# Kernel tuning notes

Measured on AMD Instinct MI355X. Metric: run time of the kernel, lower is better.

## Reference

```python
import jax, jax.numpy as jnp
import numpy as np

WINDOW = 128  # local attention window (non-overlapping blocks)
LN_EPS = 1e-5


def setup_inputs() -> dict:
    key = jax.random.key(0)
    ks = jax.random.split(key, 7)
    B, S, D = 8, 8192, 128
    scale = 1.0 / np.sqrt(D)
    x = jax.random.normal(ks[0], (B, S, D), dtype=jnp.float32)
    Wq = jax.random.normal(ks[1], (D, D), dtype=jnp.float32) * scale
    Wk = jax.random.normal(ks[2], (D, D), dtype=jnp.float32) * scale
    Wv = jax.random.normal(ks[3], (D, D), dtype=jnp.float32) * scale
    Wo = jax.random.normal(ks[4], (D, D), dtype=jnp.float32) * scale
    gamma = jnp.ones((D,), dtype=jnp.float32)
    beta = jnp.zeros((D,), dtype=jnp.float32)
    return {"x": x, "Wq": Wq, "Wk": Wk, "Wv": Wv, "Wo": Wo,
            "gamma": gamma, "beta": beta}


def _local_attention(xc, Wq, Wk, Wv, Wo):
    # xc: [B, L, D]; non-overlapping block-local attention, window=WINDOW
    B, L, D = xc.shape
    nb = L // WINDOW
    q = (xc @ Wq).reshape(B, nb, WINDOW, D)
    k = (xc @ Wk).reshape(B, nb, WINDOW, D)
    v = (xc @ Wv).reshape(B, nb, WINDOW, D)
    scores = jnp.einsum('bnwd,bnud->bnwu', q, k) / jnp.sqrt(
        jnp.asarray(D, xc.dtype))
    attn = jax.nn.softmax(scores, axis=-1)
    out = jnp.einsum('bnwu,bnud->bnwd', attn, v).reshape(B, L, D)
    return out @ Wo


def reference(x, Wq, Wk, Wv, Wo, gamma, beta):
    # passer starts as zeros_like(x); concat along seq dim doubles length
    xc = jnp.concatenate([x, jnp.zeros_like(x)], axis=1)  # [B, 2S, D]
    h = _local_attention(xc, Wq, Wk, Wv, Wo)
    # LayerNorm over last dim (learned affine)
    mu = jnp.mean(h, axis=-1, keepdims=True)
    var = jnp.mean(jnp.square(h - mu), axis=-1, keepdims=True)
    y = (h - mu) * jax.lax.rsqrt(var + LN_EPS) * gamma + beta
    # torch nn.GELU default is exact (erf) variant
    return jax.nn.gelu(y, approximate=False)
```

## Files before the change

kernel.cpp:

```cpp
#include <hip/hip_runtime.h>
#include <hip/hip_bf16.h>
#include <math.h>

using bf16 = __hip_bfloat16;
typedef short short8 __attribute__((ext_vector_type(8)));
typedef short short4v __attribute__((ext_vector_type(4)));
typedef float f32x4 __attribute__((ext_vector_type(4)));

#define MFMA16 __builtin_amdgcn_mfma_f32_16x16x32_bf16
#define S_ 8192

__device__ __forceinline__ int sw(int r, int chunk) {
  return r * 256 + (((chunk) ^ (r & 15)) << 4);
}

__device__ __forceinline__ float gelu_exact(float y) {
  return 0.5f * y * (1.0f + erff(y * 0.70710678118654752f));
}

__device__ __forceinline__ unsigned pack2(float a, float b) {
  unsigned ra = (unsigned)__bfloat16_as_ushort(__float2bfloat16(a));
  unsigned rb = (unsigned)__bfloat16_as_ushort(__float2bfloat16(b));
  return ra | (rb << 16);
}

__global__ void transw(const float* __restrict__ wq, const float* __restrict__ wk,
                       const float* __restrict__ wv, const float* __restrict__ wo,
                       bf16* __restrict__ wt) {
  __shared__ float smf[128 * 33];
  int m = blockIdx.x >> 2, sl = blockIdx.x & 3;
  const float* W = (m == 0) ? wq : (m == 1) ? wk : (m == 2) ? wv : wo;
  for (int i = 0; i < 4; ++i) {
    int u = threadIdx.x + i * 256;
    int k = u >> 3, cg = u & 7;
    float4 v = *(const float4*)(W + k * 128 + sl * 32 + cg * 4);
    smf[k * 33 + cg * 4 + 0] = v.x;
    smf[k * 33 + cg * 4 + 1] = v.y;
    smf[k * 33 + cg * 4 + 2] = v.z;
    smf[k * 33 + cg * 4 + 3] = v.w;
  }
  __syncthreads();
  for (int i = 0; i < 2; ++i) {
    int f = threadIdx.x + i * 256;
    int l15 = f & 15, q = (f >> 4) & 3, t = (f >> 6) & 3, ctl = (f >> 8) & 1;
    int ct = sl * 2 + ctl;
    int gf = ((ct * 4 + t) * 4 + q) * 16 + l15;
    int k0 = t * 32 + q * 8, nl = ctl * 16 + l15;
    bf16 tmp[8];
#pragma unroll
    for (int j = 0; j < 8; ++j)
      tmp[j] = __float2bfloat16(smf[(k0 + j) * 33 + nl]);
    *(uint4*)(wt + m * 16384 + gf * 8) = *(const uint4*)tmp;
  }
}

__device__ __forceinline__ void clr8(f32x4 acc[8]) {
#pragma unroll
  for (int j = 0; j < 8; ++j) acc[j] = (f32x4){0.f, 0.f, 0.f, 0.f};
}

__device__ __forceinline__ void mm_g(const char* tA, const char* wB, int row0,
                                     int l15, int quad, f32x4 acc[8]) {
  short8 a[4];
#pragma unroll
  for (int t = 0; t < 4; ++t)
    a[t] = *(const short8*)(tA + sw(row0 + l15, 4 * t + quad));
#pragma unroll
  for (int t = 0; t < 4; ++t) {
    short8 b[8];
#pragma unroll
    for (int ct = 0; ct < 8; ++ct)
      b[ct] = *(const short8*)(wB + ((((ct * 4 + t) * 4 + quad) * 16 + l15) << 4));
#pragma unroll
    for (int ct = 0; ct < 8; ++ct)
      acc[ct] = MFMA16(a[t], b[ct], acc[ct], 0, 0, 0);
  }
}

__device__ __forceinline__ void mm_l(const char* tA, const char* tB, int row0,
                                     int l15, int quad, f32x4 acc[8]) {
  short8 a[4];
#pragma unroll
  for (int t = 0; t < 4; ++t)
    a[t] = *(const short8*)(tA + sw(row0 + l15, 4 * t + quad));
#pragma unroll
  for (int t = 0; t < 4; ++t) {
    short8 b[8];
#pragma unroll
    for (int ct = 0; ct < 8; ++ct)
      b[ct] = *(const short8*)(tB + sw(ct * 16 + l15, 4 * t + quad));
#pragma unroll
    for (int ct = 0; ct < 8; ++ct)
      acc[ct] = MFMA16(a[t], b[ct], acc[ct], 0, 0, 0);
  }
}

__device__ __forceinline__ void store_strip(char* tile, int row0, int l15, int quad,
                                            const f32x4 acc[8], const float* rs) {
#pragma unroll
  for (int ct = 0; ct < 8; ++ct) {
    int col = ct * 16 + l15;
#pragma unroll
    for (int r = 0; r < 4; ++r) {
      int row = row0 + quad * 4 + r;
      float v = acc[ct][r];
      if (rs) v *= rs[r];
      *(bf16*)(tile + sw(row, col >> 3) + (col & 7) * 2) = __float2bfloat16(v);
    }
  }
}

__device__ __forceinline__ void stage_x_strip(char* strip, const float* xg, int lane) {
#pragma unroll
  for (int it = 0; it < 8; ++it) {
    int e = it * 256 + lane * 4;
    float4 f = *(const float4*)(xg + e);
    union { unsigned u[2]; short4v s; } pk;
    pk.u[0] = pack2(f.x, f.y);
    pk.u[1] = pack2(f.z, f.w);
    int r = e >> 7, chunk = (e >> 3) & 15, half = (lane & 1) * 8;
    *(short4v*)(strip + sw(r, chunk) + half) = pk.s;
  }
  asm volatile("" ::: "memory");
}

__global__ __launch_bounds__(512, 2) void attn_fused(
    const float* __restrict__ x, const bf16* __restrict__ wt,
    const float* __restrict__ gamma, const float* __restrict__ beta,
    float* __restrict__ out) {
  __shared__ uint4 ldsbuf[4096];
  char* t_x = (char*)ldsbuf;
  char* t_k = t_x + 32768;

  const int tid = threadIdx.x;
  const int wave = tid >> 6, lane = tid & 63;
  const int l15 = lane & 15, quad = lane >> 4;
  const int row0 = wave << 4;
  const int b = blockIdx.x >> 6, blk = blockIdx.x & 63;
  const float* xb = x + ((size_t)b * S_ + (size_t)blk * 128) * 128;
  float* outb = out + ((size_t)b * 2 * S_ + (size_t)blk * 128) * 128;

  {
    float* o2 = out + ((size_t)b * 2 * S_ + (size_t)(S_ + blk * 128)) * 128;
    int c0 = (tid * 4) & 127;
    float4 bv = *(const float4*)(beta + c0);
    float4 gv;
    gv.x = gelu_exact(bv.x); gv.y = gelu_exact(bv.y);
    gv.z = gelu_exact(bv.z); gv.w = gelu_exact(bv.w);
#pragma unroll
    for (int j = 0; j < 8; ++j)
      *(float4*)(o2 + tid * 4 + j * 2048) = gv;
  }

  stage_x_strip(t_x + wave * 4096, xb + (size_t)row0 * 128, lane);

  f32x4 acc[8];
  unsigned pV[16];

  clr8(acc);
  mm_g(t_x, (const char*)(wt + 16384), row0, l15, quad, acc);
  store_strip(t_k, row0, l15, quad, acc, nullptr);

  clr8(acc);
  mm_g(t_x, (const char*)(wt + 2 * 16384), row0, l15, quad, acc);
#pragma unroll
  for (int ct = 0; ct < 8; ++ct) {
    pV[2 * ct]     = pack2(acc[ct][0], acc[ct][1]);
    pV[2 * ct + 1] = pack2(acc[ct][2], acc[ct][3]);
  }

  clr8(acc);
  mm_g(t_x, (const char*)(wt + 0), row0, l15, quad, acc);
  store_strip(t_x, row0, l15, quad, acc, nullptr);
  __syncthreads();

  clr8(acc);
  mm_l(t_x, t_k, row0, l15, quad, acc);

  float inv[4];
  const float sscale = 0.08838834764831845f;
#pragma unroll
  for (int r = 0; r < 4; ++r) {
    float sum = 0.f;
#pragma unroll
    for (int ct = 0; ct < 8; ++ct) {
      float v = __expf(acc[ct][r] * sscale);
      acc[ct][r] = v;
      sum += v;
    }
#pragma unroll
    for (int off = 8; off; off >>= 1) sum += __shfl_xor(sum, off, 64);
    inv[r] = 1.0f / sum;
  }
  store_strip(t_x, row0, l15, quad, acc, nullptr);
  __syncthreads();

  {
    int seq = row0 + quad * 4;
#pragma unroll
    for (int ct = 0; ct < 8; ++ct) {
      int d = ct * 16 + l15;
      unsigned p[2] = {pV[2 * ct], pV[2 * ct + 1]};
      *(uint2*)(t_k + sw(d, seq >> 3) + (seq & 7) * 2) = *(const uint2*)p;
    }
  }
  __syncthreads();

  clr8(acc);
  mm_l(t_x, t_k, row0, l15, quad, acc);
  store_strip(t_x, row0, l15, quad, acc, inv);

  clr8(acc);
  mm_g(t_x, (const char*)(wt + 3 * 16384), row0, l15, quad, acc);

  float mean[4], rstd[4];
#pragma unroll
  for (int r = 0; r < 4; ++r) {
    float sum = 0.f;
#pragma unroll
    for (int ct = 0; ct < 8; ++ct) sum += acc[ct][r];
#pragma unroll
    for (int off = 8; off; off >>= 1) sum += __shfl_xor(sum, off, 64);
    mean[r] = sum * (1.0f / 128.0f);
    float sq = 0.f;
#pragma unroll
    for (int ct = 0; ct < 8; ++ct) { float d = acc[ct][r] - mean[r]; sq += d * d; }
#pragma unroll
    for (int off = 8; off; off >>= 1) sq += __shfl_xor(sq, off, 64);
    rstd[r] = rsqrtf(sq * (1.0f / 128.0f) + 1e-5f);
  }

  float gg[8], bbv[8];
#pragma unroll
  for (int ct = 0; ct < 8; ++ct) {
    gg[ct] = gamma[ct * 16 + l15];
    bbv[ct] = beta[ct * 16 + l15];
  }

  float* fs = (float*)(t_x + wave * 4096);
#pragma unroll
  for (int p = 0; p < 2; ++p) {
    asm volatile("" ::: "memory");
#pragma unroll
    for (int rr = 0; rr < 2; ++rr) {
      int r = 2 * p + rr;
      int s = quad * 2 + rr;
#pragma unroll
      for (int ct = 0; ct < 8; ++ct) {
        float y = (acc[ct][r] - mean[r]) * rstd[r] * gg[ct] + bbv[ct];
        fs[s * 128 + ct * 16 + l15] = gelu_exact(y);
      }
    }
    asm volatile("" ::: "memory");
#pragma unroll
    for (int j = 0; j < 4; ++j) {
      int u = j * 64 + lane;
      int s2 = u >> 5, coff = (u & 31) * 4;
      int grow = row0 + (s2 >> 1) * 4 + 2 * p + (s2 & 1);
      *(float4*)(outb + (size_t)grow * 128 + coff) = *(const float4*)(fs + s2 * 128 + coff);
    }
  }
}

extern "C" void kernel_launch(void* const* d_in, const int* in_sizes, int n_in,
                              void* d_out, int out_size, void* d_ws, size_t ws_size,
                              hipStream_t stream) {
  const float* x     = (const float*)d_in[0];
  const float* wq    = (const float*)d_in[1];
  const float* wk    = (const float*)d_in[2];
  const float* wv    = (const float*)d_in[3];
  const float* wo    = (const float*)d_in[4];
  const float* gamma = (const float*)d_in[5];
  const float* beta  = (const float*)d_in[6];
  float* out = (float*)d_out;
  bf16* wt  = (bf16*)d_ws;

  transw<<<16, 256, 0, stream>>>(wq, wk, wv, wo, wt);
  attn_fused<<<512, 512, 0, stream>>>(x, wt, gamma, beta, out);
}
```

Before: 148.3 us.

## Process two windows per block with LDS-staged weights and 32-row wave strips

Each block now handles two 128-row windows (256 blocks instead of 512), and each wave computes two 16-row strips. Every weight fragment is loaded once and reused across both strips. Weight matrices are staged into LDS with async global_load_lds, and x is loaded straight into registers rather than through an LDS staging pass. The goal is to cut weight fetches from global memory and raise MFMA reuse per B-fragment. In exchange, LDS grows to 160KB and register pressure rises, which lowers occupancy and adds extra barriers around the weight staging.

```diff
diff --git a/kernel.cpp b/kernel.cpp
--- a/kernel.cpp
+++ b/kernel.cpp
@@ -4,7 +4,6 @@
 
 using bf16 = __hip_bfloat16;
 typedef short short8 __attribute__((ext_vector_type(8)));
-typedef short short4v __attribute__((ext_vector_type(4)));
 typedef float f32x4 __attribute__((ext_vector_type(4)));
 
 #define MFMA16 __builtin_amdgcn_mfma_f32_16x16x32_bf16
@@ -22,6 +21,18 @@
   unsigned ra = (unsigned)__bfloat16_as_ushort(__float2bfloat16(a));
   unsigned rb = (unsigned)__bfloat16_as_ushort(__float2bfloat16(b));
   return ra | (rb << 16);
+}
+
+__device__ __forceinline__ void gl_lds16(const char* g, char* l) {
+  __builtin_amdgcn_global_load_lds(
+      (const __attribute__((address_space(1))) void*)g,
+      (__attribute__((address_space(3))) void*)l, 16, 0, 0);
+}
+
+__device__ __forceinline__ void stage_w(const char* g, char* l, int tid) {
+#pragma unroll
+  for (int i = 0; i < 4; ++i)
+    gl_lds16(g + i * 8192 + tid * 16, l + i * 8192 + tid * 16);
 }
 
 __global__ void transw(const float* __restrict__ wq, const float* __restrict__ wk,
@@ -59,207 +70,254 @@
   for (int j = 0; j < 8; ++j) acc[j] = (f32x4){0.f, 0.f, 0.f, 0.f};
 }
 
-__device__ __forceinline__ void mm_g(const char* tA, const char* wB, int row0,
-                                     int l15, int quad, f32x4 acc[8]) {
-  short8 a[4];
-#pragma unroll
-  for (int t = 0; t < 4; ++t)
-    a[t] = *(const short8*)(tA + sw(row0 + l15, 4 * t + quad));
+__device__ __forceinline__ void mm_w2(const short8 a0[4], const short8 a1[4],
+                                      const char* Wb, int l15, int quad,
+                                      f32x4 accA[8], f32x4 accB[8]) {
 #pragma unroll
   for (int t = 0; t < 4; ++t) {
-    short8 b[8];
+    short8 bfr[8];
 #pragma unroll
     for (int ct = 0; ct < 8; ++ct)
-      b[ct] = *(const short8*)(wB + ((((ct * 4 + t) * 4 + quad) * 16 + l15) << 4));
+      bfr[ct] = *(const short8*)(Wb + ((((ct * 4 + t) * 4 + quad) * 16 + l15) << 4));
+#pragma unroll
+    for (int ct = 0; ct < 8; ++ct) {
+      accA[ct] = MFMA16(a0[t], bfr[ct], accA[ct], 0, 0, 0);
+      accB[ct] = MFMA16(a1[t], bfr[ct], accB[ct], 0, 0, 0);
+    }
+  }
+}
+
+__device__ __forceinline__ void mm_sw2(const char* sA, const char* sB, const char* Wb,
+                                       int l15, int quad, f32x4 accA[8], f32x4 accB[8]) {
+#pragma unroll
+  for (int t = 0; t < 4; ++t) {
+    short8 a0 = *(const short8*)(sA + sw(l15, 4 * t + quad));
+    short8 a1 = *(const short8*)(sB + sw(l15, 4 * t + quad));
+    short8 bfr[8];
 #pragma unroll
     for (int ct = 0; ct < 8; ++ct)
-      acc[ct] = MFMA16(a[t], b[ct], acc[ct], 0, 0, 0);
-  }
-}
-
-__device__ __forceinline__ void mm_l(const char* tA, const char* tB, int row0,
-                                     int l15, int quad, f32x4 acc[8]) {
-  short8 a[4];
-#pragma unroll
-  for (int t = 0; t < 4; ++t)
-    a[t] = *(const short8*)(tA + sw(row0 + l15, 4 * t + quad));
+      bfr[ct] = *(const short8*)(Wb + ((((ct * 4 + t) * 4 + quad) * 16 + l15) << 4));
+#pragma unroll
+    for (int ct = 0; ct < 8; ++ct) {
+      accA[ct] = MFMA16(a0, bfr[ct], accA[ct], 0, 0, 0);
+      accB[ct] = MFMA16(a1, bfr[ct], accB[ct], 0, 0, 0);
+    }
+  }
+}
+
+__device__ __forceinline__ void mm_l2(const char* sA, const char* sB, const char* tB,
+                                      int l15, int quad, f32x4 accA[8], f32x4 accB[8]) {
 #pragma unroll
   for (int t = 0; t < 4; ++t) {
-    short8 b[8];
+    short8 a0 = *(const short8*)(sA + sw(l15, 4 * t + quad));
+    short8 a1 = *(const short8*)(sB + sw(l15, 4 * t + quad));
+    short8 bfr[8];
 #pragma unroll
     for (int ct = 0; ct < 8; ++ct)
-      b[ct] = *(const short8*)(tB + sw(ct * 16 + l15, 4 * t + quad));
-#pragma unroll
-    for (int ct = 0; ct < 8; ++ct)
-      acc[ct] = MFMA16(a[t], b[ct], acc[ct], 0, 0, 0);
-  }
-}
-
-__device__ __forceinline__ void store_strip(char* tile, int row0, int l15, int quad,
-                                            const f32x4 acc[8], const float* rs) {
+      bfr[ct] = *(const short8*)(tB + sw(ct * 16 + l15, 4 * t + quad));
+#pragma unroll
+    for (int ct = 0; ct < 8; ++ct) {
+      accA[ct] = MFMA16(a0, bfr[ct], accA[ct], 0, 0, 0);
+      accB[ct] = MFMA16(a1, bfr[ct], accB[ct], 0, 0, 0);
+    }
+  }
+}
+
+__device__ __forceinline__ void store_strip16(char* tile, int l15, int quad,
+                                              const f32x4 acc[8], const float* rs) {
 #pragma unroll
   for (int ct = 0; ct < 8; ++ct) {
     int col = ct * 16 + l15;
 #pragma unroll
     for (int r = 0; r < 4; ++r) {
-      int row = row0 + quad * 4 + r;
       float v = acc[ct][r];
       if (rs) v *= rs[r];
-      *(bf16*)(tile + sw(row, col >> 3) + (col & 7) * 2) = __float2bfloat16(v);
-    }
-  }
-}
-
-__device__ __forceinline__ void stage_x_strip(char* strip, const float* xg, int lane) {
-#pragma unroll
-  for (int it = 0; it < 8; ++it) {
-    int e = it * 256 + lane * 4;
-    float4 f = *(const float4*)(xg + e);
-    union { unsigned u[2]; short4v s; } pk;
-    pk.u[0] = pack2(f.x, f.y);
-    pk.u[1] = pack2(f.z, f.w);
-    int r = e >> 7, chunk = (e >> 3) & 15, half = (lane & 1) * 8;
-    *(short4v*)(strip + sw(r, chunk) + half) = pk.s;
-  }
-  asm volatile("" ::: "memory");
+      *(bf16*)(tile + sw(quad * 4 + r, col >> 3) + (col & 7) * 2) = __float2bfloat16(v);
+    }
+  }
+}
+
+__device__ __forceinline__ void softmax_rows(f32x4 acc[8], float inv[4]) {
+  const float sscale = 0.08838834764831845f;
+#pragma unroll
+  for (int r = 0; r < 4; ++r) {
+    float sum = 0.f;
+#pragma unroll
+    for (int ct = 0; ct < 8; ++ct) {
+      float v = __expf(acc[ct][r] * sscale);
+      acc[ct][r] = v;
+      sum += v;
+    }
+#pragma unroll
+    for (int off = 8; off; off >>= 1) sum += __shfl_xor(sum, off, 64);
+    inv[r] = 1.0f / sum;
+  }
+}
+
+__device__ __forceinline__ void ln_gelu_store(const f32x4 acc[8], char* strip,
+                                              float* outrow, int l15, int quad,
+                                              const float gg[8], const float bb[8]) {
+  float mean[4], rstd[4];
+#pragma unroll
+  for (int r = 0; r < 4; ++r) {
+    float sum = 0.f;
+#pragma unroll
+    for (int ct = 0; ct < 8; ++ct) sum += acc[ct][r];
+#pragma unroll
+    for (int off = 8; off; off >>= 1) sum += __shfl_xor(sum, off, 64);
+    mean[r] = sum * (1.0f / 128.0f);
+    float sq = 0.f;
+#pragma unroll
+    for (int ct = 0; ct < 8; ++ct) { float d = acc[ct][r] - mean[r]; sq += d * d; }
+#pragma unroll
+    for (int off = 8; off; off >>= 1) sq += __shfl_xor(sq, off, 64);
+    rstd[r] = rsqrtf(sq * (1.0f / 128.0f) + 1e-5f);
+  }
+  float* fs = (float*)strip;
+  const int lane = quad * 16 + l15;
+#pragma unroll
+  for (int p = 0; p < 2; ++p) {
+    asm volatile("" ::: "memory");
+#pragma unroll
+    for (int rr = 0; rr < 2; ++rr) {
+      int r = 2 * p + rr;
+      int s = quad * 2 + rr;
+#pragma unroll
+      for (int ct = 0; ct < 8; ++ct) {
+        float y = (acc[ct][r] - mean[r]) * rstd[r] * gg[ct] + bb[ct];
+        fs[s * 128 + ct * 16 + l15] = gelu_exact(y);
+      }
+    }
+    asm volatile("" ::: "memory");
+#pragma unroll
+    for (int j = 0; j < 4; ++j) {
+      int u = j * 64 + lane;
+      int s2 = u >> 5, coff = (u & 31) * 4;
+      int grow = (s2 >> 1) * 4 + 2 * p + (s2 & 1);
+      *(float4*)(outrow + (size_t)grow * 128 + coff) = *(const float4*)(fs + s2 * 128 + coff);
+    }
+  }
 }
 
 __global__ __launch_bounds__(512, 2) void attn_fused(
     const float* __restrict__ x, const bf16* __restrict__ wt,
     const float* __restrict__ gamma, const float* __restrict__ beta,
     float* __restrict__ out) {
-  __shared__ uint4 ldsbuf[4096];
-  char* t_x = (char*)ldsbuf;
-  char* t_k = t_x + 32768;
+  __shared__ uint4 ldsbuf[10240];
+  char* lds = (char*)ldsbuf;
+  char* t_s = lds;
+  char* t_k = lds + 65536;
+  char* t_w = lds + 131072;
 
   const int tid = threadIdx.x;
   const int wave = tid >> 6, lane = tid & 63;
   const int l15 = lane & 15, quad = lane >> 4;
-  const int row0 = wave << 4;
-  const int b = blockIdx.x >> 6, blk = blockIdx.x & 63;
-  const float* xb = x + ((size_t)b * S_ + (size_t)blk * 128) * 128;
-  float* outb = out + ((size_t)b * 2 * S_ + (size_t)blk * 128) * 128;
-
+  const int win = wave >> 2, widx = wave & 3;
+  const int b = blockIdx.x >> 5, sb = blockIdx.x & 31;
+
+  char* myk = t_k + win * 32768;
+  char* s0 = t_s + wave * 8192;
+  char* s1 = s0 + 4096;
+  const int r0 = widx * 32;
+  const int localrow = win * 128 + r0;
+
+  const float* xb = x + ((size_t)b * S_ + (size_t)sb * 256) * 128;
+  float* outb = out + ((size_t)b * 2 * S_ + (size_t)sb * 256) * 128;
+
+  stage_w((const char*)wt, t_w, tid);
+  short8 ax0[4], ax1[4];
   {
-    float* o2 = out + ((size_t)b * 2 * S_ + (size_t)(S_ + blk * 128)) * 128;
+    const float* xr0 = xb + (size_t)(localrow + l15) * 128 + quad * 8;
+    const float* xr1 = xr0 + 16 * 128;
+#pragma unroll
+    for (int t = 0; t < 4; ++t) {
+      float4 f0 = *(const float4*)(xr0 + t * 32);
+      float4 f1 = *(const float4*)(xr0 + t * 32 + 4);
+      float4 f2 = *(const float4*)(xr1 + t * 32);
+      float4 f3 = *(const float4*)(xr1 + t * 32 + 4);
+      union { unsigned u[4]; short8 s; } pa, pb;
+      pa.u[0] = pack2(f0.x, f0.y); pa.u[1] = pack2(f0.z, f0.w);
+      pa.u[2] = pack2(f1.x, f1.y); pa.u[3] = pack2(f1.z, f1.w);
+      pb.u[0] = pack2(f2.x, f2.y); pb.u[1] = pack2(f2.z, f2.w);
+      pb.u[2] = pack2(f3.x, f3.y); pb.u[3] = pack2(f3.z, f3.w);
+      ax0[t] = pa.s; ax1[t] = pb.s;
+    }
+  }
+  __syncthreads();
+
+  f32x4 accA[8], accB[8];
+
+  clr8(accA); clr8(accB);
+  mm_w2(ax0, ax1, t_w, l15, quad, accA, accB);
+  store_strip16(s0, l15, quad, accA, nullptr);
+  store_strip16(s1, l15, quad, accB, nullptr);
+  __syncthreads();
+
+  stage_w((const char*)(wt + 16384), t_w, tid);
+  {
+    float* o2 = out + ((size_t)b * 2 * S_ + (size_t)(S_ + sb * 256)) * 128;
     int c0 = (tid * 4) & 127;
     float4 bv = *(const float4*)(beta + c0);
     float4 gv;
     gv.x = gelu_exact(bv.x); gv.y = gelu_exact(bv.y);
     gv.z = gelu_exact(bv.z); gv.w = gelu_exact(bv.w);
 #pragma unroll
-    for (int j = 0; j < 8; ++j)
+    for (int j = 0; j < 16; ++j)
       *(float4*)(o2 + tid * 4 + j * 2048) = gv;
   }
-
-  stage_x_strip(t_x + wave * 4096, xb + (size_t)row0 * 128, lane);
-
-  f32x4 acc[8];
-  unsigned pV[16];
-
-  clr8(acc);
-  mm_g(t_x, (const char*)(wt + 16384), row0, l15, quad, acc);
-  store_strip(t_k, row0, l15, quad, acc, nullptr);
-
-  clr8(acc);
-  mm_g(t_x, (const char*)(wt + 2 * 16384), row0, l15, quad, acc);
-#pragma unroll
-  for (int ct = 0; ct < 8; ++ct) {
-    pV[2 * ct]     = pack2(acc[ct][0], acc[ct][1]);
-    pV[2 * ct + 1] = pack2(acc[ct][2], acc[ct][3]);
-  }
-
-  clr8(acc);
-  mm_g(t_x, (const char*)(wt + 0), row0, l15, quad, acc);
-  store_strip(t_x, row0, l15, quad, acc, nullptr);
-  __syncthreads();
-
-  clr8(acc);
-  mm_l(t_x, t_k, row0, l15, quad, acc);
-
-  float inv[4];
-  const float sscale = 0.08838834764831845f;
-#pragma unroll
-  for (int r = 0; r < 4; ++r) {
-    float sum = 0.f;
-#pragma unroll
-    for (int ct = 0; ct < 8; ++ct) {
-      float v = __expf(acc[ct][r] * sscale);
-      acc[ct][r] = v;
-      sum += v;
-    }
-#pragma unroll
-    for (int off = 8; off; off >>= 1) sum += __shfl_xor(sum, off, 64);
-    inv[r] = 1.0f / sum;
-  }
-  store_strip(t_x, row0, l15, quad, acc, nullptr);
-  __syncthreads();
-
+  __syncthreads();
+
+  clr8(accA); clr8(accB);
+  mm_w2(ax0, ax1, t_w, l15, quad, accA, accB);
+  store_strip16(myk + r0 * 256, l15, quad, accA, nullptr);
+  store_strip16(myk + (r0 + 16) * 256, l15, quad, accB, nullptr);
+  __syncthreads();
+
+  stage_w((const char*)(wt + 2 * 16384), t_w, tid);
+  clr8(accA); clr8(accB);
+  mm_l2(s0, s1, myk, l15, quad, accA, accB);
+  float inv0[4], inv1[4];
+  softmax_rows(accA, inv0);
+  softmax_rows(accB, inv1);
+  store_strip16(s0, l15, quad, accA, nullptr);
+  store_strip16(s1, l15, quad, accB, nullptr);
+  __syncthreads();
+
+  clr8(accA); clr8(accB);
+  mm_w2(ax0, ax1, t_w, l15, quad, accA, accB);
   {
-    int seq = row0 + quad * 4;
+    int seq0 = r0 + quad * 4;
+    int seq1 = r0 + 16 + quad * 4;
 #pragma unroll
     for (int ct = 0; ct < 8; ++ct) {
       int d = ct * 16 + l15;
-      unsigned p[2] = {pV[2 * ct], pV[2 * ct + 1]};
-      *(uint2*)(t_k + sw(d, seq >> 3) + (seq & 7) * 2) = *(const uint2*)p;
-    }
-  }
-  __syncthreads();
-
-  clr8(acc);
-  mm_l(t_x, t_k, row0, l15, quad, acc);
-  store_strip(t_x, row0, l15, quad, acc, inv);
-
-  clr8(acc);
-  mm_g(t_x, (const char*)(wt + 3 * 16384), row0, l15, quad, acc);
-
-  float mean[4], rstd[4];
-#pragma unroll
-  for (int r = 0; r < 4; ++r) {
-    float sum = 0.f;
-#pragma unroll
-    for (int ct = 0; ct < 8; ++ct) sum += acc[ct][r];
-#pragma unroll
-    for (int off = 8; off; off >>= 1) sum += __shfl_xor(sum, off, 64);
-    mean[r] = sum * (1.0f / 128.0f);
-    float sq = 0.f;
-#pragma unroll
-    for (int ct = 0; ct < 8; ++ct) { float d = acc[ct][r] - mean[r]; sq += d * d; }
-#pragma unroll
-    for (int off = 8; off; off >>= 1) sq += __shfl_xor(sq, off, 64);
-    rstd[r] = rsqrtf(sq * (1.0f / 128.0f) + 1e-5f);
-  }
-
-  float gg[8], bbv[8];
+      unsigned pa[2] = {pack2(accA[ct][0], accA[ct][1]),
+                        pack2(accA[ct][2], accA[ct][3])};
+      unsigned pb[2] = {pack2(accB[ct][0], accB[ct][1]),
+                        pack2(accB[ct][2], accB[ct][3])};
+      *(uint2*)(myk + sw(d, seq0 >> 3) + (seq0 & 7) * 2) = *(const uint2*)pa;
+      *(uint2*)(myk + sw(d, seq1 >> 3) + (seq1 & 7) * 2) = *(const uint2*)pb;
+    }
+  }
+  __syncthreads();
+
+  stage_w((const char*)(wt + 3 * 16384), t_w, tid);
+  clr8(accA); clr8(accB);
+  mm_l2(s0, s1, myk, l15, quad, accA, accB);
+  store_strip16(s0, l15, quad, accA, inv0);
+  store_strip16(s1, l15, quad, accB, inv1);
+  __syncthreads();
+
+  clr8(accA); clr8(accB);
+  mm_sw2(s0, s1, t_w, l15, quad, accA, accB);
+  float gg[8], bb[8];
 #pragma unroll
   for (int ct = 0; ct < 8; ++ct) {
     gg[ct] = gamma[ct * 16 + l15];
-    bbv[ct] = beta[ct * 16 + l15];
-  }
-
-  float* fs = (float*)(t_x + wave * 4096);
-#pragma unroll
-  for (int p = 0; p < 2; ++p) {
-    asm volatile("" ::: "memory");
-#pragma unroll
-    for (int rr = 0; rr < 2; ++rr) {
-      int r = 2 * p + rr;
-      int s = quad * 2 + rr;
-#pragma unroll
-      for (int ct = 0; ct < 8; ++ct) {
-        float y = (acc[ct][r] - mean[r]) * rstd[r] * gg[ct] + bbv[ct];
-        fs[s * 128 + ct * 16 + l15] = gelu_exact(y);
-      }
-    }
-    asm volatile("" ::: "memory");
-#pragma unroll
-    for (int j = 0; j < 4; ++j) {
-      int u = j * 64 + lane;
-      int s2 = u >> 5, coff = (u & 31) * 4;
-      int grow = row0 + (s2 >> 1) * 4 + 2 * p + (s2 & 1);
-      *(float4*)(outb + (size_t)grow * 128 + coff) = *(const float4*)(fs + s2 * 128 + coff);
-    }
-  }
+    bb[ct] = beta[ct * 16 + l15];
+  }
+  ln_gelu_store(accA, s0, outb + (size_t)localrow * 128, l15, quad, gg, bb);
+  ln_gelu_store(accB, s1, outb + (size_t)(localrow + 16) * 128, l15, quad, gg, bb);
 }
 
 extern "C" void kernel_launch(void* const* d_in, const int* in_sizes, int n_in,
@@ -276,5 +334,5 @@
   bf16* wt  = (bf16*)d_ws;
 
   transw<<<16, 256, 0, stream>>>(wq, wk, wv, wo, wt);
-  attn_fused<<<512, 512, 0, stream>>>(x, wt, gamma, beta, out);
-}
+  attn_fused<<<256, 512, 0, stream>>>(x, wt, gamma, beta, out);
+}
```

Result: faster. 124.4 us, median of 3 (-16.1%).
